# Kernel tuning notes

Measured on AMD Instinct MI355X. Metric: run time of the kernel, lower is better.

## Reference

```python
import jax, jax.numpy as jnp
import numpy as np
from jax import lax

CHUNK = 256  # points of the query set processed per step; intermediate is [B, CHUNK, M]


def _nn_min(x, y):
    """For each point in x [B,N,3], squared distance + index of nearest point in y [B,M,3].
    Chunked over N so the full [B,N,M] distance matrix is never materialized."""
    B, N, _ = x.shape
    y2 = jnp.sum(y * y, axis=-1)  # [B, M]
    K = N // CHUNK
    xr = jnp.swapaxes(x.reshape(B, K, CHUNK, 3), 0, 1)  # [K, B, CHUNK, 3]

    def chunk_fn(xc):  # xc: [B, CHUNK, 3]
        d = (jnp.sum(xc * xc, axis=-1)[..., None]
             - 2.0 * jnp.einsum('bcd,bmd->bcm', xc, y)
             + y2[:, None, :])  # [B, CHUNK, M]
        return jnp.min(d, axis=-1), jnp.argmin(d, axis=-1).astype(jnp.int32)

    dmin, idx = lax.map(chunk_fn, xr)  # [K, B, CHUNK]
    dmin = jnp.swapaxes(dmin, 0, 1).reshape(B, N)
    idx = jnp.swapaxes(idx, 0, 1).reshape(B, N)
    return dmin, idx


def setup_inputs() -> dict:
    key = jax.random.key(0)
    k1, k2 = jax.random.split(key)
    xyz1 = jax.random.normal(k1, (8, 16384, 3), dtype=jnp.float32)
    xyz2 = jax.random.normal(k2, (8, 16384, 3), dtype=jnp.float32)
    return {"xyz1": xyz1, "xyz2": xyz2}


def reference(xyz1, xyz2):
    dist1, idx1 = _nn_min(xyz1, xyz2)  # [B, N], [B, N]
    dist2, idx2 = _nn_min(xyz2, xyz1)  # [B, M], [B, M]
    return dist1, dist2, idx1, idx2
```

## Files before the change

kernel.cpp:

```cpp
#include <hip/hip_runtime.h>
#include <stdint.h>

#define BATCH 8
#define NPTS  16384
#define BN    (BATCH * NPTS)
#define CH    512
#define NCH   (NPTS / CH)
#define QPB   256
#define MARGIN 1.0e-2f

typedef float f32x16 __attribute__((ext_vector_type(16)));
typedef short s16x8  __attribute__((ext_vector_type(8)));

__device__ __forceinline__ uint16_t bfr(float x) {
    uint32_t u = __float_as_uint(x);
    return (uint16_t)((u + 0x7FFFu + ((u >> 16) & 1u)) >> 16);
}
__device__ __forceinline__ float bff(uint16_t s) {
    return __uint_as_float(((uint32_t)s) << 16);
}
__device__ __forceinline__ void split2(float v, uint16_t* a, uint16_t* b) {
    *a = bfr(v); *b = bfr(v - bff(*a));
}
__device__ __forceinline__ uint32_t pk2(uint16_t lo, uint16_t hi) {
    return (uint32_t)lo | ((uint32_t)hi << 16);
}

#define F16(M_) M_(0) M_(1) M_(2) M_(3) M_(4) M_(5) M_(6) M_(7) \
                M_(8) M_(9) M_(10) M_(11) M_(12) M_(13) M_(14) M_(15)

#define MIN3(a, b, c) fminf(fminf((a), (b)), (c))

__device__ __forceinline__ float fold16(const f32x16 a) {
    const float u0 = MIN3(a[0],  a[1],  a[2]);
    const float u1 = MIN3(a[3],  a[4],  a[5]);
    const float u2 = MIN3(a[6],  a[7],  a[8]);
    const float u3 = MIN3(a[9],  a[10], a[11]);
    const float u4 = MIN3(a[12], a[13], a[14]);
    const float v0 = MIN3(u0, u1, a[15]);
    const float v1 = MIN3(u2, u3, u4);
    return fminf(v0, v1);
}

__global__ __launch_bounds__(256) void enc_kernel(
    const float* __restrict__ Y, uint4* __restrict__ enc)
{
#pragma clang fp contract(off)
    const int g = blockIdx.x * 256 + threadIdx.x;
    const int b = g >> 14, p = g & (NPTS - 1);
    const float y0 = Y[(size_t)g * 3 + 0];
    const float y1 = Y[(size_t)g * 3 + 1];
    const float y2 = Y[(size_t)g * 3 + 2];
    const float ys = (y0 * y0 + y1 * y1) + y2 * y2;
    uint16_t Ya, Yb; split2(ys, &Ya, &Yb);
    uint16_t H0, M0; split2(-2.0f * y0, &H0, &M0);
    uint16_t H1, M1; split2(-2.0f * y1, &H1, &M1);
    uint16_t H2, M2; split2(-2.0f * y2, &H2, &M2);
    const uint16_t ONE = 0x3F80;
    const int ch = p >> 9, pp = p & (CH - 1);
    const size_t base = (size_t)(b * NCH + ch) * (2 * CH) + pp;
    enc[base]      = make_uint4(pk2(ONE, ONE), pk2(Ya, Yb), pk2(H0, M0), pk2(H0, M0));
    enc[base + CH] = make_uint4(pk2(H1, M1), pk2(H1, M1), pk2(H2, M2), pk2(H2, M2));
}

#define DECODE_DBX() \
    int dir, batch, xblk; \
    { const int g = blockIdx.x; \
      if (ndir == 2) { const int s = 2 * (g & 7) + ((g >> 3) & 1); \
          dir = s >> 3; batch = s & 7; xblk = g >> 4; } \
      else { dir = dir0; batch = g & 7; xblk = g >> 3; } }

#define STAGE(c, buf) { \
        const uint4* src_ = ep + (size_t)(c) * (2 * CH); \
        _Pragma("unroll") \
        for (int i_ = 0; i_ < 4; ++i_) \
            __builtin_amdgcn_global_load_lds( \
                (const __attribute__((address_space(1))) void*)(src_ + i_ * 256 + tid), \
                (__attribute__((address_space(3))) void*)&lds[buf][i_ * 256 + tid], \
                16, 0, 0); \
    }

#define MKQFR(dst, qq, qx0v, qx1v, qx2v, qxsv) { \
        const float* xp = Xp + (size_t)(bofs + (qq)) * 3; \
        qx0v = xp[0]; qx1v = xp[1]; qx2v = xp[2]; \
        qxsv = (qx0v * qx0v + qx1v * qx1v) + qx2v * qx2v; \
        uint16_t Xa, Xb; split2(qxsv, &Xa, &Xb); \
        uint16_t h0, m0; split2(qx0v, &h0, &m0); \
        uint16_t h1, m1; split2(qx1v, &h1, &m1); \
        uint16_t h2, m2; split2(qx2v, &h2, &m2); \
        const uint16_t ONE = 0x3F80; \
        if (hi == 0) { \
            dst[0]=(short)Xa; dst[1]=(short)Xb; dst[2]=(short)ONE; dst[3]=(short)ONE; \
            dst[4]=(short)h0; dst[5]=(short)h0; dst[6]=(short)m0;  dst[7]=(short)m0; \
        } else { \
            dst[0]=(short)h1; dst[1]=(short)h1; dst[2]=(short)m1;  dst[3]=(short)m1; \
            dst[4]=(short)h2; dst[5]=(short)h2; dst[6]=(short)m2;  dst[7]=(short)m2; \
        } }

__global__ __launch_bounds__(256, 4) void nn_sweep1(
    const float* __restrict__ xyz1, const float* __restrict__ xyz2,
    const uint4* __restrict__ encA, const uint4* __restrict__ encB,
    float* __restrict__ mprime, int ndir, int dir0)
{
#pragma clang fp contract(off)
    __shared__ uint4 lds[2][2 * CH];

    const int tid = threadIdx.x;
    const int l   = tid & 63;
    const int wv  = tid >> 6;
    const int col = l & 31;
    const int hi  = l >> 5;
    DECODE_DBX()

    const float* Xp = dir ? xyz2 : xyz1;
    const uint4* ep = (dir ? encB : encA) + (size_t)batch * (NCH * 2 * CH);
    const int bofs  = batch * NPTS;
    const int qbase = xblk * QPB + wv * 64;

    const f32x16 zf = {0.f,0.f,0.f,0.f,0.f,0.f,0.f,0.f,
                       0.f,0.f,0.f,0.f,0.f,0.f,0.f,0.f};

    s16x8 qfr0, qfr1;
    float qa0, qa1, qa2, qas, qb0, qb1, qb2, qbs;
    MKQFR(qfr0, qbase + col,      qa0, qa1, qa2, qas)
    MKQFR(qfr1, qbase + 32 + col, qb0, qb1, qb2, qbs)
    (void)qa0; (void)qb0;

    const int ldsb = hi * CH + col;

    float run0 = __builtin_inff(), run1 = __builtin_inff();
    STAGE(0, 0);
    __syncthreads();
    int cur = 0;
    for (int c = 0; c < NCH; ++c) {
        if (c + 1 < NCH) STAGE(c + 1, cur ^ 1);
#pragma unroll
        for (int tp = 0; tp < CH / 64; ++tp) {
            const s16x8 pA = *(const s16x8*)&lds[cur][ldsb + (2 * tp) * 32];
            const s16x8 pB = *(const s16x8*)&lds[cur][ldsb + (2 * tp + 1) * 32];
            const f32x16 a0 = __builtin_amdgcn_mfma_f32_32x32x16_bf16(pA, qfr0, zf, 0, 0, 0);
            const f32x16 a1 = __builtin_amdgcn_mfma_f32_32x32x16_bf16(pA, qfr1, zf, 0, 0, 0);
            const f32x16 a2 = __builtin_amdgcn_mfma_f32_32x32x16_bf16(pB, qfr0, zf, 0, 0, 0);
            const f32x16 a3 = __builtin_amdgcn_mfma_f32_32x32x16_bf16(pB, qfr1, zf, 0, 0, 0);
            run0 = MIN3(run0, fold16(a0), fold16(a2));
            run1 = MIN3(run1, fold16(a1), fold16(a3));
        }
        __syncthreads();
        cur ^= 1;
    }
    run0 = fminf(run0, __shfl_xor(run0, 32, 64));
    run1 = fminf(run1, __shfl_xor(run1, 32, 64));
    if (l < 32) {
        float* mp = mprime + (size_t)dir * BN + bofs + qbase;
        mp[col]      = run0;
        mp[32 + col] = run1;
    }
}

__global__ __launch_bounds__(256, 4) void nn_sweep2(
    const float* __restrict__ xyz1, const float* __restrict__ xyz2,
    const uint4* __restrict__ encA, const uint4* __restrict__ encB,
    const float* __restrict__ mprime, float* __restrict__ out,
    int ndir, int dir0)
{
#pragma clang fp contract(off)
    __shared__ uint4 lds[2][2 * CH];
    __shared__ unsigned long long keys[QPB];

    const int tid = threadIdx.x;
    const int l   = tid & 63;
    const int wv  = tid >> 6;
    const int col = l & 31;
    const int hi  = l >> 5;
    DECODE_DBX()

    const float* Xp = dir ? xyz2 : xyz1;
    const float* Yp = dir ? xyz1 : xyz2;
    const uint4* ep = (dir ? encB : encA) + (size_t)batch * (NCH * 2 * CH);
    const int bofs  = batch * NPTS;
    const int qbase = xblk * QPB + wv * 64;

    keys[tid] = ~0ull;

    const f32x16 zf = {0.f,0.f,0.f,0.f,0.f,0.f,0.f,0.f,
                       0.f,0.f,0.f,0.f,0.f,0.f,0.f,0.f};

    int rowpack[4] = {0, 0, 0, 0};
    {
        s16x8 pa = {0,0,0,0,0,0,0,0}, pb = {0,0,0,0,0,0,0,0};
        if (hi == 0) { pa[0] = (short)bfr((float)col); pb[0] = (short)0x3F80; }
        const f32x16 rowp = __builtin_amdgcn_mfma_f32_32x32x16_bf16(pa, pb, zf, 0, 0, 0);
#define PR(i) rowpack[(i) >> 2] |= ((int)rowp[i] & 0xFF) << (((i) & 3) * 8);
        F16(PR)
#undef PR
    }

    s16x8 qfr0, qfr1;
    float qa0, qa1, qa2, qas, qb0, qb1, qb2, qbs;
    MKQFR(qfr0, qbase + col,      qa0, qa1, qa2, qas)
    MKQFR(qfr1, qbase + 32 + col, qb0, qb1, qb2, qbs)

    float thr0, thr1;
    {
        const float* mp = mprime + (size_t)dir * BN + bofs + qbase;
        thr0 = mp[col] + MARGIN;
        thr1 = mp[32 + col] + MARGIN;
    }

    const int ldsb = hi * CH + col;

#define HITR(accv, jb, foff, thr, qx0, qx1, qx2, qxs, r) \
        if ((accv)[r] <= (thr)) { \
            const int jc = (jb) + ((rowpack[(r) >> 2] >> (((r) & 3) * 8)) & 0xFF); \
            const float* yq = Yp + (size_t)(bofs + jc) * 3; \
            const float py0 = yq[0], py1 = yq[1], py2 = yq[2]; \
            const float pys = (py0 * py0 + py1 * py1) + py2 * py2; \
            const float dd = ((qxs) - 2.0f * (((qx0) * py0 + (qx1) * py1) + (qx2) * py2)) + pys; \
            uint32_t kb = __float_as_uint(dd); \
            kb = (kb & 0x80000000u) ? ~kb : (kb | 0x80000000u); \
            atomicMin(&keys[wv * 64 + (foff) + col], \
                      ((unsigned long long)kb << 32) | (uint32_t)jc); }
#define HIT(accv, jb, foff, thr, qx0, qx1, qx2, qxs) \
        if (fold16(accv) <= (thr)) { \
            HITR(accv, jb, foff, thr, qx0, qx1, qx2, qxs, 0) \
            HITR(accv, jb, foff, thr, qx0, qx1, qx2, qxs, 1) \
            HITR(accv, jb, foff, thr, qx0, qx1, qx2, qxs, 2) \
            HITR(accv, jb, foff, thr, qx0, qx1, qx2, qxs, 3) \
            HITR(accv, jb, foff, thr, qx0, qx1, qx2, qxs, 4) \
            HITR(accv, jb, foff, thr, qx0, qx1, qx2, qxs, 5) \
            HITR(accv, jb, foff, thr, qx0, qx1, qx2, qxs, 6) \
            HITR(accv, jb, foff, thr, qx0, qx1, qx2, qxs, 7) \
            HITR(accv, jb, foff, thr, qx0, qx1, qx2, qxs, 8) \
            HITR(accv, jb, foff, thr, qx0, qx1, qx2, qxs, 9) \
            HITR(accv, jb, foff, thr, qx0, qx1, qx2, qxs, 10) \
            HITR(accv, jb, foff, thr, qx0, qx1, qx2, qxs, 11) \
            HITR(accv, jb, foff, thr, qx0, qx1, qx2, qxs, 12) \
            HITR(accv, jb, foff, thr, qx0, qx1, qx2, qxs, 13) \
            HITR(accv, jb, foff, thr, qx0, qx1, qx2, qxs, 14) \
            HITR(accv, jb, foff, thr, qx0, qx1, qx2, qxs, 15) \
        }

    STAGE(0, 0);
    __syncthreads();
    int cur = 0;
    for (int c = 0; c < NCH; ++c) {
        if (c + 1 < NCH) STAGE(c + 1, cur ^ 1);
#pragma unroll
        for (int tp = 0; tp < CH / 64; ++tp) {
            const s16x8 pA = *(const s16x8*)&lds[cur][ldsb + (2 * tp) * 32];
            const s16x8 pB = *(const s16x8*)&lds[cur][ldsb + (2 * tp + 1) * 32];
            const int jbA = c * CH + (2 * tp) * 32;
            {
                const f32x16 a0 = __builtin_amdgcn_mfma_f32_32x32x16_bf16(pA, qfr0, zf, 0, 0, 0);
                const f32x16 a2 = __builtin_amdgcn_mfma_f32_32x32x16_bf16(pB, qfr0, zf, 0, 0, 0);
                HIT(a0, jbA,      0, thr0, qa0, qa1, qa2, qas)
                HIT(a2, jbA + 32, 0, thr0, qa0, qa1, qa2, qas)
            }
            {
                const f32x16 a1 = __builtin_amdgcn_mfma_f32_32x32x16_bf16(pA, qfr1, zf, 0, 0, 0);
                const f32x16 a3 = __builtin_amdgcn_mfma_f32_32x32x16_bf16(pB, qfr1, zf, 0, 0, 0);
                HIT(a1, jbA,      32, thr1, qb0, qb1, qb2, qbs)
                HIT(a3, jbA + 32, 32, thr1, qb0, qb1, qb2, qbs)
            }
        }
        __syncthreads();
        cur ^= 1;
    }
#undef HIT
#undef HITR

    __syncthreads();
    {
        const unsigned long long m = keys[tid];
        const uint32_t k32 = (uint32_t)(m >> 32);
        const uint32_t db  = (k32 & 0x80000000u) ? (k32 ^ 0x80000000u) : ~k32;
        const size_t gq = (size_t)bofs + (size_t)xblk * QPB + tid;
        float* distp = out + (size_t)dir * BN;
        float* idxp  = out + (size_t)(2 + dir) * BN;
        distp[gq] = __uint_as_float(db);
        idxp[gq]  = (float)(uint32_t)(m & 0xFFFFFFFFu);
    }
}

extern "C" void kernel_launch(void* const* d_in, const int* in_sizes, int n_in,
                              void* d_out, int out_size, void* d_ws, size_t ws_size,
                              hipStream_t stream) {
    const float* xyz1 = (const float*)d_in[0];
    const float* xyz2 = (const float*)d_in[1];
    float* out = (float*)d_out;

    uint4* encA   = (uint4*)d_ws;
    uint4* encB   = encA + (size_t)BN * 2;
    float* mpri   = (float*)(encB + (size_t)BN * 2);

    if (ws_size >= (size_t)10 * 1024 * 1024) {
        enc_kernel<<<BN / 256, 256, 0, stream>>>(xyz2, encA);
        enc_kernel<<<BN / 256, 256, 0, stream>>>(xyz1, encB);
        nn_sweep1<<<1024, 256, 0, stream>>>(xyz1, xyz2, encA, encB, mpri, 2, 0);
        nn_sweep2<<<1024, 256, 0, stream>>>(xyz1, xyz2, encA, encB, mpri, out, 2, 0);
    } else {
        float* mp2 = (float*)(encA + (size_t)BN * 2);
        enc_kernel<<<BN / 256, 256, 0, stream>>>(xyz2, encA);
        nn_sweep1<<<512, 256, 0, stream>>>(xyz1, xyz2, encA, encA, mp2, 1, 0);
        nn_sweep2<<<512, 256, 0, stream>>>(xyz1, xyz2, encA, encA, mp2, out, 1, 0);
        enc_kernel<<<BN / 256, 256, 0, stream>>>(xyz1, encA);
        nn_sweep1<<<512, 256, 0, stream>>>(xyz1, xyz2, encA, encA, mp2, 1, 1);
        nn_sweep2<<<512, 256, 0, stream>>>(xyz1, xyz2, encA, encA, mp2, out, 1, 1);
    }
}
```

Baseline: 408.2 us.

## Split candidate range across two blocks with atomic key merging

Each query block's sweep over the candidate set is split in two halves handled by separate blocks (2048 blocks instead of 1024). Partial minima are merged with global atomicMin on order-preserving keys, and a new writeout kernel decodes the merged keys. The chunk size is halved to 256 so the LDS footprint per block drops, and the refinement margin is tightened so fewer candidates are re-checked exactly. This adds a memset, global atomics and an extra launch in exchange for more parallelism and occupancy, and the smaller margin risks missing true nearest neighbours.

```diff
diff --git a/kernel.cpp b/kernel.cpp
--- a/kernel.cpp
+++ b/kernel.cpp
@@ -4,10 +4,10 @@
 #define BATCH 8
 #define NPTS  16384
 #define BN    (BATCH * NPTS)
-#define CH    512
+#define CH    256
 #define NCH   (NPTS / CH)
 #define QPB   256
-#define MARGIN 1.0e-2f
+#define MARGIN 4.0e-3f
 
 typedef float f32x16 __attribute__((ext_vector_type(16)));
 typedef short s16x8  __attribute__((ext_vector_type(8)));
@@ -24,6 +24,13 @@
 }
 __device__ __forceinline__ uint32_t pk2(uint16_t lo, uint16_t hi) {
     return (uint32_t)lo | ((uint32_t)hi << 16);
+}
+__device__ __forceinline__ uint32_t key32(float d) {
+    uint32_t b = __float_as_uint(d);
+    return (b & 0x80000000u) ? ~b : (b | 0x80000000u);
+}
+__device__ __forceinline__ float dec32(uint32_t k) {
+    return __uint_as_float((k & 0x80000000u) ? (k ^ 0x80000000u) : ~k);
 }
 
 #define F16(M_) M_(0) M_(1) M_(2) M_(3) M_(4) M_(5) M_(6) M_(7) \
@@ -57,23 +64,24 @@
     uint16_t H1, M1; split2(-2.0f * y1, &H1, &M1);
     uint16_t H2, M2; split2(-2.0f * y2, &H2, &M2);
     const uint16_t ONE = 0x3F80;
-    const int ch = p >> 9, pp = p & (CH - 1);
+    const int ch = p >> 8, pp = p & (CH - 1);
     const size_t base = (size_t)(b * NCH + ch) * (2 * CH) + pp;
     enc[base]      = make_uint4(pk2(ONE, ONE), pk2(Ya, Yb), pk2(H0, M0), pk2(H0, M0));
     enc[base + CH] = make_uint4(pk2(H1, M1), pk2(H1, M1), pk2(H2, M2), pk2(H2, M2));
 }
 
 #define DECODE_DBX() \
-    int dir, batch, xblk; \
+    int dir, batch, kh, xblk; \
     { const int g = blockIdx.x; \
-      if (ndir == 2) { const int s = 2 * (g & 7) + ((g >> 3) & 1); \
-          dir = s >> 3; batch = s & 7; xblk = g >> 4; } \
-      else { dir = dir0; batch = g & 7; xblk = g >> 3; } }
+      const int s = 2 * (g & 7) + ((g >> 3) & 1); \
+      dir = s >> 3; batch = s & 7; \
+      if (ksplit == 2) { kh = (g >> 4) & 1; xblk = g >> 5; } \
+      else             { kh = 0;            xblk = g >> 4; } }
 
 #define STAGE(c, buf) { \
         const uint4* src_ = ep + (size_t)(c) * (2 * CH); \
         _Pragma("unroll") \
-        for (int i_ = 0; i_ < 4; ++i_) \
+        for (int i_ = 0; i_ < 2; ++i_) \
             __builtin_amdgcn_global_load_lds( \
                 (const __attribute__((address_space(1))) void*)(src_ + i_ * 256 + tid), \
                 (__attribute__((address_space(3))) void*)&lds[buf][i_ * 256 + tid], \
@@ -100,7 +108,7 @@
 __global__ __launch_bounds__(256, 4) void nn_sweep1(
     const float* __restrict__ xyz1, const float* __restrict__ xyz2,
     const uint4* __restrict__ encA, const uint4* __restrict__ encB,
-    float* __restrict__ mprime, int ndir, int dir0)
+    uint32_t* __restrict__ mkey, int ksplit)
 {
 #pragma clang fp contract(off)
     __shared__ uint4 lds[2][2 * CH];
@@ -116,6 +124,8 @@
     const uint4* ep = (dir ? encB : encA) + (size_t)batch * (NCH * 2 * CH);
     const int bofs  = batch * NPTS;
     const int qbase = xblk * QPB + wv * 64;
+    const int chalf = NCH / ksplit;
+    const int c0 = kh * chalf, c1 = c0 + chalf;
 
     const f32x16 zf = {0.f,0.f,0.f,0.f,0.f,0.f,0.f,0.f,
                        0.f,0.f,0.f,0.f,0.f,0.f,0.f,0.f};
@@ -129,11 +139,11 @@
     const int ldsb = hi * CH + col;
 
     float run0 = __builtin_inff(), run1 = __builtin_inff();
-    STAGE(0, 0);
+    STAGE(c0, 0);
     __syncthreads();
     int cur = 0;
-    for (int c = 0; c < NCH; ++c) {
-        if (c + 1 < NCH) STAGE(c + 1, cur ^ 1);
+    for (int c = c0; c < c1; ++c) {
+        if (c + 1 < c1) STAGE(c + 1, cur ^ 1);
 #pragma unroll
         for (int tp = 0; tp < CH / 64; ++tp) {
             const s16x8 pA = *(const s16x8*)&lds[cur][ldsb + (2 * tp) * 32];
@@ -151,17 +161,17 @@
     run0 = fminf(run0, __shfl_xor(run0, 32, 64));
     run1 = fminf(run1, __shfl_xor(run1, 32, 64));
     if (l < 32) {
-        float* mp = mprime + (size_t)dir * BN + bofs + qbase;
-        mp[col]      = run0;
-        mp[32 + col] = run1;
+        uint32_t* mp = mkey + (size_t)dir * BN + bofs + qbase;
+        atomicMin(&mp[col],      key32(run0));
+        atomicMin(&mp[32 + col], key32(run1));
     }
 }
 
 __global__ __launch_bounds__(256, 4) void nn_sweep2(
     const float* __restrict__ xyz1, const float* __restrict__ xyz2,
     const uint4* __restrict__ encA, const uint4* __restrict__ encB,
-    const float* __restrict__ mprime, float* __restrict__ out,
-    int ndir, int dir0)
+    const uint32_t* __restrict__ mkey, unsigned long long* __restrict__ gkeys,
+    float* __restrict__ out, int ksplit)
 {
 #pragma clang fp contract(off)
     __shared__ uint4 lds[2][2 * CH];
@@ -179,6 +189,8 @@
     const uint4* ep = (dir ? encB : encA) + (size_t)batch * (NCH * 2 * CH);
     const int bofs  = batch * NPTS;
     const int qbase = xblk * QPB + wv * 64;
+    const int chalf = NCH / ksplit;
+    const int c0 = kh * chalf, c1 = c0 + chalf;
 
     keys[tid] = ~0ull;
 
@@ -202,9 +214,9 @@
 
     float thr0, thr1;
     {
-        const float* mp = mprime + (size_t)dir * BN + bofs + qbase;
-        thr0 = mp[col] + MARGIN;
-        thr1 = mp[32 + col] + MARGIN;
+        const uint32_t* mp = mkey + (size_t)dir * BN + bofs + qbase;
+        thr0 = dec32(mp[col]) + MARGIN;
+        thr1 = dec32(mp[32 + col]) + MARGIN;
     }
 
     const int ldsb = hi * CH + col;
@@ -216,10 +228,8 @@
             const float py0 = yq[0], py1 = yq[1], py2 = yq[2]; \
             const float pys = (py0 * py0 + py1 * py1) + py2 * py2; \
             const float dd = ((qxs) - 2.0f * (((qx0) * py0 + (qx1) * py1) + (qx2) * py2)) + pys; \
-            uint32_t kb = __float_as_uint(dd); \
-            kb = (kb & 0x80000000u) ? ~kb : (kb | 0x80000000u); \
             atomicMin(&keys[wv * 64 + (foff) + col], \
-                      ((unsigned long long)kb << 32) | (uint32_t)jc); }
+                      ((unsigned long long)key32(dd) << 32) | (uint32_t)jc); }
 #define HIT(accv, jb, foff, thr, qx0, qx1, qx2, qxs) \
         if (fold16(accv) <= (thr)) { \
             HITR(accv, jb, foff, thr, qx0, qx1, qx2, qxs, 0) \
@@ -240,11 +250,11 @@
             HITR(accv, jb, foff, thr, qx0, qx1, qx2, qxs, 15) \
         }
 
-    STAGE(0, 0);
+    STAGE(c0, 0);
     __syncthreads();
     int cur = 0;
-    for (int c = 0; c < NCH; ++c) {
-        if (c + 1 < NCH) STAGE(c + 1, cur ^ 1);
+    for (int c = c0; c < c1; ++c) {
+        if (c + 1 < c1) STAGE(c + 1, cur ^ 1);
 #pragma unroll
         for (int tp = 0; tp < CH / 64; ++tp) {
             const s16x8 pA = *(const s16x8*)&lds[cur][ldsb + (2 * tp) * 32];
@@ -272,14 +282,27 @@
     __syncthreads();
     {
         const unsigned long long m = keys[tid];
-        const uint32_t k32 = (uint32_t)(m >> 32);
-        const uint32_t db  = (k32 & 0x80000000u) ? (k32 ^ 0x80000000u) : ~k32;
-        const size_t gq = (size_t)bofs + (size_t)xblk * QPB + tid;
-        float* distp = out + (size_t)dir * BN;
-        float* idxp  = out + (size_t)(2 + dir) * BN;
-        distp[gq] = __uint_as_float(db);
-        idxp[gq]  = (float)(uint32_t)(m & 0xFFFFFFFFu);
-    }
+        const size_t gq = (size_t)dir * BN + bofs + (size_t)xblk * QPB + tid;
+        if (ksplit == 2) {
+            atomicMin(&gkeys[gq], m);
+        } else {
+            const uint32_t k32 = (uint32_t)(m >> 32);
+            const size_t q = (size_t)bofs + (size_t)xblk * QPB + tid;
+            out[(size_t)dir * BN + q]       = dec32(k32);
+            out[(size_t)(2 + dir) * BN + q] = (float)(uint32_t)(m & 0xFFFFFFFFu);
+        }
+    }
+}
+
+__global__ __launch_bounds__(256) void writeout_k(
+    const unsigned long long* __restrict__ gkeys, float* __restrict__ out)
+{
+    const size_t i = (size_t)blockIdx.x * 256 + threadIdx.x;
+    const unsigned long long m = gkeys[i];
+    const int dir = (int)(i / BN);
+    const size_t q = i - (size_t)dir * BN;
+    out[(size_t)dir * BN + q]       = dec32((uint32_t)(m >> 32));
+    out[(size_t)(2 + dir) * BN + q] = (float)(uint32_t)(m & 0xFFFFFFFFu);
 }
 
 extern "C" void kernel_launch(void* const* d_in, const int* in_sizes, int n_in,
@@ -289,22 +312,22 @@
     const float* xyz2 = (const float*)d_in[1];
     float* out = (float*)d_out;
 
-    uint4* encA   = (uint4*)d_ws;
-    uint4* encB   = encA + (size_t)BN * 2;
-    float* mpri   = (float*)(encB + (size_t)BN * 2);
-
-    if (ws_size >= (size_t)10 * 1024 * 1024) {
-        enc_kernel<<<BN / 256, 256, 0, stream>>>(xyz2, encA);
-        enc_kernel<<<BN / 256, 256, 0, stream>>>(xyz1, encB);
-        nn_sweep1<<<1024, 256, 0, stream>>>(xyz1, xyz2, encA, encB, mpri, 2, 0);
-        nn_sweep2<<<1024, 256, 0, stream>>>(xyz1, xyz2, encA, encB, mpri, out, 2, 0);
+    uint4*    encA  = (uint4*)d_ws;
+    uint4*    encB  = encA + (size_t)BN * 2;
+    uint32_t* mkey  = (uint32_t*)(encB + (size_t)BN * 2);
+    unsigned long long* gkeys = (unsigned long long*)(mkey + (size_t)2 * BN);
+
+    enc_kernel<<<BN / 256, 256, 0, stream>>>(xyz2, encA);
+    enc_kernel<<<BN / 256, 256, 0, stream>>>(xyz1, encB);
+
+    if (ws_size >= (size_t)11 * 1024 * 1024) {
+        hipMemsetAsync(mkey, 0xFF, (size_t)3 * 1024 * 1024, stream);
+        nn_sweep1<<<2048, 256, 0, stream>>>(xyz1, xyz2, encA, encB, mkey, 2);
+        nn_sweep2<<<2048, 256, 0, stream>>>(xyz1, xyz2, encA, encB, mkey, gkeys, out, 2);
+        writeout_k<<<(2 * BN) / 256, 256, 0, stream>>>(gkeys, out);
     } else {
-        float* mp2 = (float*)(encA + (size_t)BN * 2);
-        enc_kernel<<<BN / 256, 256, 0, stream>>>(xyz2, encA);
-        nn_sweep1<<<512, 256, 0, stream>>>(xyz1, xyz2, encA, encA, mp2, 1, 0);
-        nn_sweep2<<<512, 256, 0, stream>>>(xyz1, xyz2, encA, encA, mp2, out, 1, 0);
-        enc_kernel<<<BN / 256, 256, 0, stream>>>(xyz1, encA);
-        nn_sweep1<<<512, 256, 0, stream>>>(xyz1, xyz2, encA, encA, mp2, 1, 1);
-        nn_sweep2<<<512, 256, 0, stream>>>(xyz1, xyz2, encA, encA, mp2, out, 1, 1);
-    }
-}
+        hipMemsetAsync(mkey, 0xFF, (size_t)1024 * 1024, stream);
+        nn_sweep1<<<1024, 256, 0, stream>>>(xyz1, xyz2, encA, encB, mkey, 1);
+        nn_sweep2<<<1024, 256, 0, stream>>>(xyz1, xyz2, encA, encB, mkey, nullptr, out, 1);
+    }
+}
```

Measured after the change: 372.2 us. 8.8% less time.
